# Kernel optimization log

Hardware: AMD Instinct MI355X
Metric: run time of the kernel (lower is better)

The kernel has to match this reference:

```python
import jax, jax.numpy as jnp
import numpy as np

N_HEADS = 16
D_HEAD = 64
D_MODEL = 1024
WINDOW = 256
B, T = 4, 2048


def rotate_half(x):
    x1, x2 = jnp.split(x, 2, axis=-1)
    return jnp.concatenate([-x2, x1], axis=-1)


def apply_rope(x, cos, sin):
    return x * cos + rotate_half(x) * sin


def setup_inputs() -> dict:
    key = jax.random.key(0)
    ks = jax.random.split(key, 5)
    x = jax.random.normal(ks[0], (B, T, D_MODEL), dtype=jnp.float32)
    cos = jax.random.normal(ks[1], (1, T, 1, D_HEAD), dtype=jnp.float32)
    sin = jax.random.normal(ks[2], (1, T, 1, D_HEAD), dtype=jnp.float32)
    qkv_w = jax.random.normal(ks[3], (3 * D_MODEL, D_MODEL), dtype=jnp.float32) * (D_MODEL ** -0.5)
    out_w = jax.random.normal(ks[4], (D_MODEL, D_MODEL), dtype=jnp.float32) * (D_MODEL ** -0.5)
    return {"x": x, "cos": cos, "sin": sin, "qkv_w": qkv_w, "out_w": out_w}


def reference(x, cos, sin, qkv_w, out_w):
    Bc, Tc, C = x.shape
    # QKV projection (bias-free Linear: y = x @ W^T)
    qkv = jnp.einsum('btc,fc->btf', x, qkv_w)
    q, k, v = jnp.split(qkv, 3, axis=-1)
    # [B, H, T, d]
    def to_heads(t):
        return t.reshape(Bc, Tc, N_HEADS, D_HEAD).transpose(0, 2, 1, 3)
    q, k, v = to_heads(q), to_heads(k), to_heads(v)
    # RoPE: cos/sin [1, T, 1, d] -> [1, 1, T, d] broadcasting over heads
    cos_t = cos[:, :Tc].transpose(0, 2, 1, 3)
    sin_t = sin[:, :Tc].transpose(0, 2, 1, 3)
    q = apply_rope(q, cos_t, sin_t)
    k = apply_rope(k, cos_t, sin_t)
    # banded causal mask: allow j <= i and j >= i - (window-1)
    i = jnp.arange(Tc)[:, None]
    j = jnp.arange(Tc)[None, :]
    allowed = (j <= i) & (j >= i - (WINDOW - 1))  # [T, T]
    scale = 1.0 / jnp.sqrt(jnp.asarray(D_HEAD, dtype=q.dtype))
    scores = jnp.einsum('bhqd,bhkd->bhqk', q, k) * scale
    scores = jnp.where(allowed[None, None], scores, jnp.finfo(scores.dtype).min)
    attn = jax.nn.softmax(scores, axis=-1)
    out = jnp.einsum('bhqk,bhkd->bhqd', attn, v)
    out = out.transpose(0, 2, 1, 3).reshape(Bc, Tc, C)
    return jnp.einsum('btc,oc->bto', out, out_w)
```

## Files before the change

kernel.cpp:

```cpp
#include <hip/hip_runtime.h>

typedef __bf16 bf16_t;
typedef __bf16 bf16x8 __attribute__((ext_vector_type(8)));
typedef __bf16 bf16x4 __attribute__((ext_vector_type(4)));
typedef float f32x4 __attribute__((ext_vector_type(4)));

#define GLOAD_LDS16(gptr, lptr)                                                              \
  __builtin_amdgcn_global_load_lds((const __attribute__((address_space(1))) void*)(gptr),    \
                                   (__attribute__((address_space(3))) void*)(lptr), 16, 0, 0)

__device__ __forceinline__ f32x4 f32x4_zero() {
  f32x4 v; v[0] = 0.f; v[1] = 0.f; v[2] = 0.f; v[3] = 0.f; return v;
}

__global__ void cast3_kernel(const float* __restrict__ a, const float* __restrict__ b,
                             const float* __restrict__ c, bf16_t* __restrict__ oa,
                             bf16_t* __restrict__ ob, bf16_t* __restrict__ oc) {
  int i = blockIdx.x * blockDim.x + threadIdx.x;
  const float* src; bf16_t* dst; int j;
  if (i < 2097152) { src = a; dst = oa; j = i; }
  else if (i < 2883584) { src = b; dst = ob; j = i - 2097152; }
  else { src = c; dst = oc; j = i - 2883584; }
  float4 v = ((const float4*)src)[j];
  bf16x4 o;
  o[0] = (bf16_t)v.x; o[1] = (bf16_t)v.y; o[2] = (bf16_t)v.z; o[3] = (bf16_t)v.w;
  ((bf16x4*)dst)[j] = o;
}

#define GT_AELE 16384
#define GT_BELE 8192
#define GT_TILE (GT_AELE + GT_BELE)

__device__ __forceinline__ void gt_stage(const bf16_t* __restrict__ A,
                                         const bf16_t* __restrict__ B, bf16_t* buf,
                                         int bm, int bn, int t, int K, int tid) {
#pragma unroll
  for (int i = 0; i < 4; i++) {
    int gi = tid + i * 512;
    int row = gi >> 3, g = gi & 7;
    const bf16_t* src = A + (size_t)(bm * 256 + row) * K + t * 64 + ((g ^ (row & 7)) << 3);
    GLOAD_LDS16(src, buf + gi * 8);
  }
#pragma unroll
  for (int i = 0; i < 2; i++) {
    int gi = tid + i * 512;
    int row = gi >> 3, g = gi & 7;
    const bf16_t* src = B + (size_t)(bn * 128 + row) * K + t * 64 + ((g ^ (row & 7)) << 3);
    GLOAD_LDS16(src, buf + GT_AELE + gi * 8);
  }
}

template <int MODE>
__global__ __launch_bounds__(512, 1) void gemm_bt_kernel(
    const bf16_t* __restrict__ A, const bf16_t* __restrict__ B, float* __restrict__ C,
    bf16_t* __restrict__ oq, bf16_t* __restrict__ ok_, bf16_t* __restrict__ ov,
    const float* __restrict__ cosp, const float* __restrict__ sinp,
    int M, int N, int K) {
  __shared__ bf16_t lds[3 * GT_TILE];

  const int tid = threadIdx.x;
  const int lane = tid & 63;
  const int wid = tid >> 6;
  const int wr = wid >> 1;
  const int wc = wid & 1;
  const int l16 = lane & 15;
  const int qd = lane >> 4;
  const int bm = blockIdx.x, bn = blockIdx.y;

  f32x4 acc[4][4];
#pragma unroll
  for (int m = 0; m < 4; m++)
#pragma unroll
    for (int n = 0; n < 4; n++) acc[m][n] = f32x4_zero();

  const int NT = K >> 6;

  gt_stage(A, B, lds, bm, bn, 0, K, tid);
  gt_stage(A, B, lds + GT_TILE, bm, bn, 1, K, tid);
  asm volatile("s_waitcnt vmcnt(6)" ::: "memory");
  __builtin_amdgcn_s_barrier();
  __builtin_amdgcn_sched_barrier(0);

  int s = 0;
  for (int j = 0; j < NT; ++j) {
    if (j + 2 < NT) {
      int s2 = s + 2; if (s2 >= 3) s2 -= 3;
      gt_stage(A, B, lds + s2 * GT_TILE, bm, bn, j + 2, K, tid);
    }

    const bf16_t* bufc = lds + s * GT_TILE;
    bf16x8 af[4][2], bf[4][2];
#pragma unroll
    for (int m = 0; m < 4; m++)
#pragma unroll
      for (int kk = 0; kk < 2; kk++) {
        int row = wr * 64 + m * 16 + l16;
        af[m][kk] = *(const bf16x8*)&bufc[row * 64 + (((kk * 4 + qd) ^ (row & 7)) << 3)];
      }
#pragma unroll
    for (int n = 0; n < 4; n++)
#pragma unroll
      for (int kk = 0; kk < 2; kk++) {
        int row = wc * 64 + n * 16 + l16;
        bf[n][kk] = *(const bf16x8*)&bufc[GT_AELE + row * 64 + (((kk * 4 + qd) ^ (row & 7)) << 3)];
      }

    __builtin_amdgcn_s_setprio(1);
#pragma unroll
    for (int m = 0; m < 4; m++)
#pragma unroll
      for (int n = 0; n < 4; n++)
#pragma unroll
        for (int kk = 0; kk < 2; kk++)
          acc[m][n] = __builtin_amdgcn_mfma_f32_16x16x32_bf16(af[m][kk], bf[n][kk], acc[m][n], 0, 0, 0);
    __builtin_amdgcn_s_setprio(0);

    if (j + 2 < NT) {
      asm volatile("s_waitcnt vmcnt(6)" ::: "memory");
    } else {
      asm volatile("s_waitcnt vmcnt(0)" ::: "memory");
    }
    __builtin_amdgcn_s_barrier();
    __builtin_amdgcn_sched_barrier(0);
    s = (s == 2) ? 0 : s + 1;
  }

  if (MODE == 0) {
#pragma unroll
    for (int m = 0; m < 4; m++)
#pragma unroll
      for (int n = 0; n < 4; n++)
#pragma unroll
        for (int r = 0; r < 4; r++) {
          int row = bm * 256 + wr * 64 + m * 16 + qd * 4 + r;
          int col = bn * 128 + wc * 64 + n * 16 + l16;
          C[(size_t)row * N + col] = acc[m][n][r];
        }
  } else {
    const int colbase = bn * 128 + wc * 64;
    const int part = colbase >> 10;
    const int h = (colbase & 1023) >> 6;
    if (part == 2) {
      bf16_t* lw = lds + wid * 4096;
#pragma unroll
      for (int m = 0; m < 4; m++)
#pragma unroll
        for (int n = 0; n < 4; n++) {
          int d = n * 16 + l16;
          int gr = (m * 2 + (qd >> 1)) ^ (d & 7);
          bf16x4 w;
          w[0] = (bf16_t)acc[m][n][0];
          w[1] = (bf16_t)acc[m][n][1];
          w[2] = (bf16_t)acc[m][n][2];
          w[3] = (bf16_t)acc[m][n][3];
          *(bf16x4*)&lw[d * 64 + gr * 8 + (qd & 1) * 4] = w;
        }
      asm volatile("s_waitcnt lgkmcnt(0)" ::: "memory");
      __builtin_amdgcn_sched_barrier(0);
      const int rowbase = bm * 256 + wr * 64;
      const int bb = rowbase >> 11, tb = rowbase & 2047;
      bf16_t* vbase = ov + ((size_t)(bb * 16 + h) * 64) * 2048 + tb;
#pragma unroll
      for (int it = 0; it < 8; it++) {
        int d = it * 8 + (lane >> 3);
        int g = lane & 7;
        *(bf16x8*)&vbase[(size_t)d * 2048 + g * 8] =
            *(const bf16x8*)&lw[d * 64 + ((g ^ (d & 7)) << 3)];
      }
    } else {
      bf16_t* dst = (part == 0) ? oq : ok_;
      const float qsc = (part == 0) ? 0.18033688011112042f : 1.0f;
#pragma unroll
      for (int m = 0; m < 4; m++)
#pragma unroll
        for (int r = 0; r < 4; r++) {
          int row = bm * 256 + wr * 64 + m * 16 + qd * 4 + r;
          int b = row >> 11, t = row & 2047;
          size_t basei = (((size_t)(b * 16 + h)) * 2048 + t) * 64;
#pragma unroll
          for (int nb = 0; nb < 2; nb++) {
            int d = nb * 16 + l16;
            float xl = acc[m][nb][r];
            float xh = acc[m][nb + 2][r];
            float cl = cosp[t * 64 + d], ch = cosp[t * 64 + d + 32];
            float sl = sinp[t * 64 + d], sh = sinp[t * 64 + d + 32];
            dst[basei + d]      = (bf16_t)((xl * cl - xh * sl) * qsc);
            dst[basei + d + 32] = (bf16_t)((xh * ch + xl * sh) * qsc);
          }
        }
    }
  }
}

__global__ __launch_bounds__(256) void attn_kernel(
    const bf16_t* __restrict__ qh, const bf16_t* __restrict__ kh,
    const bf16_t* __restrict__ vt, bf16_t* __restrict__ ao) {
  __shared__ bf16_t qs[4][64 * 64];
  __shared__ bf16_t ks[2][64 * 64];
  __shared__ bf16_t vts[2][64 * 64];
  __shared__ bf16_t ps[4][16 * 64];

  const int tid = threadIdx.x;
  const int lane = tid & 63;
  const int wid = tid >> 6;
  const int l16 = lane & 15;
  const int qd = lane >> 4;

  const int bh = blockIdx.x;
  const int chunk = blockIdx.y;
  const int b = bh >> 4, h = bh & 15;

  auto swz4 = [](int f) { int r = f >> 3; return r * 8 + ((f & 7) ^ (r & 7)); };

  {
    const uint4* src = (const uint4*)(qh + ((size_t)bh * 2048 + chunk * 256) * 64);
#pragma unroll
    for (int qt = 0; qt < 4; qt++) {
      uint4* dst = (uint4*)qs[qt];
      dst[swz4(tid)] = src[qt * 512 + tid];
      dst[swz4(tid + 256)] = src[qt * 512 + tid + 256];
    }
  }

  bf16x8 bones;
#pragma unroll
  for (int e = 0; e < 8; e++) bones[e] = (bf16_t)1.0f;

  f32x4 oacc[4][4];
  float l_i[4][4];
#pragma unroll
  for (int qt = 0; qt < 4; qt++)
#pragma unroll
    for (int nb = 0; nb < 4; nb++) {
      oacc[qt][nb] = f32x4_zero();
      l_i[qt][nb] = 0.f;
    }

  const int cbase = chunk * 4;
  const int c0 = (cbase >= 4) ? cbase - 4 : 0;
  const int c1 = cbase + 3;

  for (int c = c0; c <= c1; c++) {
    const int p = c & 1;
    __syncthreads();
    {
      const uint4* ksrc = (const uint4*)(kh + ((size_t)bh * 2048 + c * 64) * 64);
      uint4* kdst = (uint4*)ks[p];
      uint4* vdst = (uint4*)vts[p];
      kdst[swz4(tid)] = ksrc[tid];
      kdst[swz4(tid + 256)] = ksrc[tid + 256];
      int f = tid;
      vdst[swz4(f)] = *(const uint4*)(vt + (size_t)(bh * 64 + (f >> 3)) * 2048 + c * 64 + (f & 7) * 8);
      f = tid + 256;
      vdst[swz4(f)] = *(const uint4*)(vt + (size_t)(bh * 64 + (f >> 3)) * 2048 + c * 64 + (f & 7) * 8);
    }
    __syncthreads();

    const int lc = c - cbase;
#pragma unroll
    for (int qt = 0; qt < 4; qt++) {
      if (qt < lc || qt > lc + 4) continue;
      const int i0q = chunk * 256 + qt * 64;

      f32x4 sacc[4];
#pragma unroll
      for (int nb = 0; nb < 4; nb++) sacc[nb] = f32x4_zero();
#pragma unroll
      for (int kk = 0; kk < 2; kk++) {
        bf16x8 afr = *(const bf16x8*)&qs[qt][(wid * 16 + l16) * 64 + (((kk * 4 + qd) ^ (l16 & 7)) * 8)];
#pragma unroll
        for (int nb = 0; nb < 4; nb++) {
          bf16x8 bfr = *(const bf16x8*)&ks[p][(nb * 16 + l16) * 64 + (((kk * 4 + qd) ^ (l16 & 7)) * 8)];
          sacc[nb] = __builtin_amdgcn_mfma_f32_16x16x32_bf16(afr, bfr, sacc[nb], 0, 0, 0);
        }
      }

#pragma unroll
      for (int r = 0; r < 4; r++) {
        const int i = i0q + wid * 16 + qd * 4 + r;
        const int prow = qd * 4 + r;
#pragma unroll
        for (int nb = 0; nb < 4; nb++) {
          const int j = c * 64 + nb * 16 + l16;
          bool valid = (j <= i) && (j + 256 > i);
          float pv = valid ? exp2f(sacc[nb][r]) : 0.f;
          ps[wid][prow * 64 + (((nb * 2 + (l16 >> 3)) ^ (prow & 7)) * 8) + (l16 & 7)] = (bf16_t)pv;
        }
      }

      asm volatile("s_waitcnt lgkmcnt(0)" ::: "memory");
      __builtin_amdgcn_sched_barrier(0);

      f32x4 lacc = f32x4_zero();
#pragma unroll
      for (int kk = 0; kk < 2; kk++) {
        bf16x8 afr = *(const bf16x8*)&ps[wid][l16 * 64 + (((kk * 4 + qd) ^ (l16 & 7)) * 8)];
        lacc = __builtin_amdgcn_mfma_f32_16x16x32_bf16(afr, bones, lacc, 0, 0, 0);
#pragma unroll
        for (int nb = 0; nb < 4; nb++) {
          bf16x8 bfr = *(const bf16x8*)&vts[p][(nb * 16 + l16) * 64 + (((kk * 4 + qd) ^ (l16 & 7)) * 8)];
          oacc[qt][nb] = __builtin_amdgcn_mfma_f32_16x16x32_bf16(afr, bfr, oacc[qt][nb], 0, 0, 0);
        }
      }
#pragma unroll
      for (int r = 0; r < 4; r++) l_i[qt][r] += lacc[r];
    }
  }

#pragma unroll
  for (int qt = 0; qt < 4; qt++)
#pragma unroll
    for (int nb = 0; nb < 4; nb++)
#pragma unroll
      for (int r = 0; r < 4; r++) {
        int t = chunk * 256 + qt * 64 + wid * 16 + qd * 4 + r;
        ao[((size_t)(b * 2048 + t)) * 1024 + h * 64 + nb * 16 + l16] =
            (bf16_t)(oacc[qt][nb][r] / l_i[qt][r]);
      }
}

extern "C" void kernel_launch(void* const* d_in, const int* in_sizes, int n_in,
                              void* d_out, int out_size, void* d_ws, size_t ws_size,
                              hipStream_t stream) {
  const float* x    = (const float*)d_in[0];
  const float* cosp = (const float*)d_in[1];
  const float* sinp = (const float*)d_in[2];
  const float* qkvw = (const float*)d_in[3];
  const float* outw = (const float*)d_in[4];
  float* out = (float*)d_out;

  char* ws = (char*)d_ws;
  bf16_t* xb  = (bf16_t*)(ws + 0);
  bf16_t* qwb = (bf16_t*)(ws + 16777216);
  bf16_t* owb = (bf16_t*)(ws + 23068672);
  bf16_t* qhp = (bf16_t*)(ws + 25165824);
  bf16_t* khp = (bf16_t*)(ws + 41943040);
  bf16_t* vtp = (bf16_t*)(ws + 58720256);
  bf16_t* aop = (bf16_t*)(ws + 75497472);

  cast3_kernel<<<12288, 256, 0, stream>>>(x, qkvw, outw, xb, qwb, owb);

  gemm_bt_kernel<1><<<dim3(32, 24), 512, 0, stream>>>(xb, qwb, nullptr, qhp, khp, vtp,
                                                      cosp, sinp, 8192, 3072, 1024);
  attn_kernel<<<dim3(64, 8), 256, 0, stream>>>(qhp, khp, vtp, aop);
  gemm_bt_kernel<0><<<dim3(32, 8), 512, 0, stream>>>(aop, owb, out, nullptr, nullptr, nullptr,
                                                     nullptr, nullptr, 8192, 1024, 1024);
}
```

Measured before the change: 209.6 us.

## Keep Q fragments in registers and prefetch next K/V tile into registers

Q fragments are now loaded straight from global memory into registers once per block, replacing the 32KB shared-memory Q tile and its per-iteration LDS reads. K and V for the next chunk are prefetched into registers while the current chunk is computed, then written to shared memory at the top of the next iteration. This hides global load latency behind the MFMA work and cuts LDS use, which may raise occupancy. The cost is extra VGPR pressure from the held Q fragments and prefetch buffers.

```diff
diff --git a/kernel.cpp b/kernel.cpp
--- a/kernel.cpp
+++ b/kernel.cpp
@@ -195,7 +195,6 @@
 __global__ __launch_bounds__(256) void attn_kernel(
     const bf16_t* __restrict__ qh, const bf16_t* __restrict__ kh,
     const bf16_t* __restrict__ vt, bf16_t* __restrict__ ao) {
-  __shared__ bf16_t qs[4][64 * 64];
   __shared__ bf16_t ks[2][64 * 64];
   __shared__ bf16_t vts[2][64 * 64];
   __shared__ bf16_t ps[4][16 * 64];
@@ -212,15 +211,13 @@
 
   auto swz4 = [](int f) { int r = f >> 3; return r * 8 + ((f & 7) ^ (r & 7)); };
 
-  {
-    const uint4* src = (const uint4*)(qh + ((size_t)bh * 2048 + chunk * 256) * 64);
-#pragma unroll
-    for (int qt = 0; qt < 4; qt++) {
-      uint4* dst = (uint4*)qs[qt];
-      dst[swz4(tid)] = src[qt * 512 + tid];
-      dst[swz4(tid + 256)] = src[qt * 512 + tid + 256];
-    }
-  }
+  bf16x8 qfr[4][2];
+#pragma unroll
+  for (int qt = 0; qt < 4; qt++)
+#pragma unroll
+    for (int kk = 0; kk < 2; kk++)
+      qfr[qt][kk] = *(const bf16x8*)(qh +
+          ((size_t)bh * 2048 + chunk * 256 + qt * 64 + wid * 16 + l16) * 64 + (kk * 4 + qd) * 8);
 
   bf16x8 bones;
 #pragma unroll
@@ -239,20 +236,33 @@
   const int cbase = chunk * 4;
   const int c0 = (cbase >= 4) ? cbase - 4 : 0;
   const int c1 = cbase + 3;
+
+  uint4 kr0, kr1, vr0, vr1;
+  {
+    const uint4* ksrc = (const uint4*)(kh + ((size_t)bh * 2048 + c0 * 64) * 64);
+    kr0 = ksrc[tid]; kr1 = ksrc[tid + 256];
+    vr0 = *(const uint4*)(vt + (size_t)(bh * 64 + (tid >> 3)) * 2048 + c0 * 64 + (tid & 7) * 8);
+    int f2 = tid + 256;
+    vr1 = *(const uint4*)(vt + (size_t)(bh * 64 + (f2 >> 3)) * 2048 + c0 * 64 + (f2 & 7) * 8);
+  }
 
   for (int c = c0; c <= c1; c++) {
     const int p = c & 1;
     __syncthreads();
     {
-      const uint4* ksrc = (const uint4*)(kh + ((size_t)bh * 2048 + c * 64) * 64);
       uint4* kdst = (uint4*)ks[p];
       uint4* vdst = (uint4*)vts[p];
-      kdst[swz4(tid)] = ksrc[tid];
-      kdst[swz4(tid + 256)] = ksrc[tid + 256];
-      int f = tid;
-      vdst[swz4(f)] = *(const uint4*)(vt + (size_t)(bh * 64 + (f >> 3)) * 2048 + c * 64 + (f & 7) * 8);
-      f = tid + 256;
-      vdst[swz4(f)] = *(const uint4*)(vt + (size_t)(bh * 64 + (f >> 3)) * 2048 + c * 64 + (f & 7) * 8);
+      kdst[swz4(tid)] = kr0;
+      kdst[swz4(tid + 256)] = kr1;
+      vdst[swz4(tid)] = vr0;
+      vdst[swz4(tid + 256)] = vr1;
+    }
+    if (c < c1) {
+      const uint4* ksrc = (const uint4*)(kh + ((size_t)bh * 2048 + (c + 1) * 64) * 64);
+      kr0 = ksrc[tid]; kr1 = ksrc[tid + 256];
+      vr0 = *(const uint4*)(vt + (size_t)(bh * 64 + (tid >> 3)) * 2048 + (c + 1) * 64 + (tid & 7) * 8);
+      int f2 = tid + 256;
+      vr1 = *(const uint4*)(vt + (size_t)(bh * 64 + (f2 >> 3)) * 2048 + (c + 1) * 64 + (f2 & 7) * 8);
     }
     __syncthreads();
 
@@ -267,11 +277,10 @@
       for (int nb = 0; nb < 4; nb++) sacc[nb] = f32x4_zero();
 #pragma unroll
       for (int kk = 0; kk < 2; kk++) {
-        bf16x8 afr = *(const bf16x8*)&qs[qt][(wid * 16 + l16) * 64 + (((kk * 4 + qd) ^ (l16 & 7)) * 8)];
 #pragma unroll
         for (int nb = 0; nb < 4; nb++) {
           bf16x8 bfr = *(const bf16x8*)&ks[p][(nb * 16 + l16) * 64 + (((kk * 4 + qd) ^ (l16 & 7)) * 8)];
-          sacc[nb] = __builtin_amdgcn_mfma_f32_16x16x32_bf16(afr, bfr, sacc[nb], 0, 0, 0);
+          sacc[nb] = __builtin_amdgcn_mfma_f32_16x16x32_bf16(qfr[qt][kk], bfr, sacc[nb], 0, 0, 0);
         }
       }
 
```

New measurement: 224.9 us. +7.3%, slower.

## Double-buffer K/V tiles in attention with async global-to-LDS loads

Applied to the files above, without the earlier changes.

The attention kernel now stages Q, K and V tiles with global_load_lds direct-to-LDS transfers instead of loading through registers and storing to LDS. The XOR swizzle moves from the LDS address to the global source address. The next K/V tile is prefetched into the alternate buffer while the current tile is computed, with one vmcnt wait and barrier per iteration replacing two syncthreads. The aim is to hide global load latency behind MFMA work and cut VGPR traffic and barriers, at the cost of relying on correct vmcnt ordering for the async LDS writes.

```diff
diff --git a/kernel.cpp b/kernel.cpp
--- a/kernel.cpp
+++ b/kernel.cpp
@@ -210,17 +210,39 @@
   const int chunk = blockIdx.y;
   const int b = bh >> 4, h = bh & 15;
 
-  auto swz4 = [](int f) { int r = f >> 3; return r * 8 + ((f & 7) ^ (r & 7)); };
+  const int f0 = tid, f1 = tid + 256;
+  const int r0 = f0 >> 3, g0 = f0 & 7;
+  const int r1 = f1 >> 3, g1 = f1 & 7;
+  const int sg0 = (g0 ^ (r0 & 7)) << 3;
+  const int sg1 = (g1 ^ (r1 & 7)) << 3;
 
   {
-    const uint4* src = (const uint4*)(qh + ((size_t)bh * 2048 + chunk * 256) * 64);
+    const bf16_t* qsrc = qh + ((size_t)bh * 2048 + chunk * 256) * 64;
 #pragma unroll
     for (int qt = 0; qt < 4; qt++) {
-      uint4* dst = (uint4*)qs[qt];
-      dst[swz4(tid)] = src[qt * 512 + tid];
-      dst[swz4(tid + 256)] = src[qt * 512 + tid + 256];
-    }
-  }
+      GLOAD_LDS16(qsrc + (size_t)(qt * 64 + r0) * 64 + sg0, &qs[qt][f0 * 8]);
+      GLOAD_LDS16(qsrc + (size_t)(qt * 64 + r1) * 64 + sg1, &qs[qt][f1 * 8]);
+    }
+  }
+
+  const int cbase = chunk * 4;
+  const int c0 = (cbase >= 4) ? cbase - 4 : 0;
+  const int c1 = cbase + 3;
+
+  const bf16_t* kbase = kh + (size_t)bh * 2048 * 64;
+  const bf16_t* vbase = vt + (size_t)bh * 64 * 2048;
+
+  auto stage_kv = [&](int c, int p) {
+    GLOAD_LDS16(kbase + (size_t)(c * 64 + r0) * 64 + sg0, &ks[p][f0 * 8]);
+    GLOAD_LDS16(kbase + (size_t)(c * 64 + r1) * 64 + sg1, &ks[p][f1 * 8]);
+    GLOAD_LDS16(vbase + (size_t)r0 * 2048 + c * 64 + sg0, &vts[p][f0 * 8]);
+    GLOAD_LDS16(vbase + (size_t)r1 * 2048 + c * 64 + sg1, &vts[p][f1 * 8]);
+  };
+
+  stage_kv(c0, c0 & 1);
+  asm volatile("s_waitcnt vmcnt(0)" ::: "memory");
+  __builtin_amdgcn_s_barrier();
+  __builtin_amdgcn_sched_barrier(0);
 
   bf16x8 bones;
 #pragma unroll
@@ -236,25 +258,9 @@
       l_i[qt][nb] = 0.f;
     }
 
-  const int cbase = chunk * 4;
-  const int c0 = (cbase >= 4) ? cbase - 4 : 0;
-  const int c1 = cbase + 3;
-
   for (int c = c0; c <= c1; c++) {
     const int p = c & 1;
-    __syncthreads();
-    {
-      const uint4* ksrc = (const uint4*)(kh + ((size_t)bh * 2048 + c * 64) * 64);
-      uint4* kdst = (uint4*)ks[p];
-      uint4* vdst = (uint4*)vts[p];
-      kdst[swz4(tid)] = ksrc[tid];
-      kdst[swz4(tid + 256)] = ksrc[tid + 256];
-      int f = tid;
-      vdst[swz4(f)] = *(const uint4*)(vt + (size_t)(bh * 64 + (f >> 3)) * 2048 + c * 64 + (f & 7) * 8);
-      f = tid + 256;
-      vdst[swz4(f)] = *(const uint4*)(vt + (size_t)(bh * 64 + (f >> 3)) * 2048 + c * 64 + (f & 7) * 8);
-    }
-    __syncthreads();
+    if (c < c1) stage_kv(c + 1, p ^ 1);
 
     const int lc = c - cbase;
 #pragma unroll
@@ -304,6 +310,12 @@
       }
 #pragma unroll
       for (int r = 0; r < 4; r++) l_i[qt][r] += lacc[r];
+    }
+
+    if (c < c1) {
+      asm volatile("s_waitcnt vmcnt(0)" ::: "memory");
+      __builtin_amdgcn_s_barrier();
+      __builtin_amdgcn_sched_barrier(0);
     }
   }
 
```

Result: no change. 212.4 us (+1.3%).
